# Kernel tuning notes

Hardware: AMD Instinct MI355X
Metric: run time of the kernel (lower is better)

The kernel has to match this reference:

```python
import jax, jax.numpy as jnp
import numpy as np

H, W, C_IN, C_OUT, N = 512, 512, 256, 256, 65536


def setup_inputs() -> dict:
    key = jax.random.key(0)
    k1, k2, k3, k4 = jax.random.split(key, 4)
    feature = jax.random.normal(k1, (1, C_IN, H, W), dtype=jnp.float32)
    weight = jax.random.normal(k2, (C_OUT, C_IN, 3, 3), dtype=jnp.float32) * 0.05
    # base sparse locations in the unpadded map; build 3x3 neighborhood indices
    # into the PADDED ([H+2, W+2]) map, exactly like F.pad + fancy indexing.
    base_h = jax.random.randint(k3, (N,), 0, H, dtype=jnp.int32)
    base_w = jax.random.randint(k4, (N,), 0, W, dtype=jnp.int32)
    dh = jnp.repeat(jnp.arange(3, dtype=jnp.int32), 3)  # [9]: 0,0,0,1,1,1,2,2,2
    dw = jnp.tile(jnp.arange(3, dtype=jnp.int32), 3)    # [9]: 0,1,2,0,1,2,...
    h_idx = base_h[None, :] + dh[:, None]  # [9, N], values in [0, H+1]
    w_idx = base_w[None, :] + dw[:, None]  # [9, N], values in [0, W+1]
    return {"feature": feature, "weight": weight, "h_idx": h_idx, "w_idx": w_idx}


def reference(feature, weight, h_idx, w_idx):
    # feature: [1, C, H, W]; weight: [Cout, C, 3, 3]; h_idx/w_idx: [9, N]
    C = feature.shape[1]
    out_ch = weight.shape[0]
    # F.pad(feature, [1,1,1,1])[0] -> [C, H+2, W+2]
    padded = jnp.pad(feature, ((0, 0), (0, 0), (1, 1), (1, 1)))[0]
    # gather 3x3 neighborhoods at sparse locations -> [C, 9, N]
    gathered = padded[:, h_idx, w_idx]
    # .view(9*C, -1): contiguous reshape gives row index c*9 + k
    g = gathered.reshape(C * 9, -1)  # [C*9, N]
    # kernel_d2s = weight.view(out, -1): row ordering c*9 + (kh*3+kw) matches
    k2d = weight.reshape(out_ch, -1)  # [Cout, C*9]
    return k2d @ g  # [Cout, N]
```

## Files before the change

kernel.cpp:

```cpp
#include <hip/hip_runtime.h>
#include <hip/hip_bf16.h>

#define HH 512
#define WW 512
#define CIN 256
#define COUT 256
#define NPTS 65536
#define PW 514
#define NPIX (PW * PW)
#define NKT 72

typedef __bf16 bf16x8 __attribute__((ext_vector_type(8)));
typedef float f32x16 __attribute__((ext_vector_type(16)));
typedef unsigned short us8 __attribute__((ext_vector_type(8)));

static __device__ __forceinline__ unsigned short f2bf(float f) {
  unsigned u = __builtin_bit_cast(unsigned, f);
  unsigned r = u + 0x7fffu + ((u >> 16) & 1u);
  return (unsigned short)(r >> 16);
}

static __device__ __forceinline__ void gload16(const void* g, void* l) {
  __builtin_amdgcn_global_load_lds(
      (const __attribute__((address_space(1))) unsigned int*)g,
      (__attribute__((address_space(3))) unsigned int*)l, 16, 0, 0);
}

__global__ __launch_bounds__(256) void prep_weight(const float* __restrict__ w,
                                                   unsigned short* __restrict__ A) {
  int i = blockIdx.x * 256 + threadIdx.x;
  int kt = i >> 13;
  int o  = i & 8191;
  int r  = o >> 5;
  int cp = (o >> 3) & 3;
  int j  = o & 7;
  int c  = cp ^ ((r >> 1) & 3);
  int k  = kt * 32 + c * 8 + j;
  int t  = k >> 8;
  int ci = k & 255;
  A[i] = f2bf(w[r * 2304 + ci * 9 + t]);
}

__global__ __launch_bounds__(256) void border_zero(unsigned short* __restrict__ Ft) {
  int g = blockIdx.x * 256 + threadIdx.x;
  if (g >= 2052 * 32) return;
  int p = g >> 5, c = g & 31;
  int py, px;
  if (p < 514)        { py = 0;        px = p; }
  else if (p < 1028)  { py = 513;      px = p - 514; }
  else if (p < 1540)  { py = p - 1027; px = 0; }
  else                { py = p - 1539; px = 513; }
  *(us8*)&Ft[((size_t)py * PW + px) * 256 + c * 8] = (us8){0, 0, 0, 0, 0, 0, 0, 0};
}

__global__ __launch_bounds__(256) void transpose_feat(const float* __restrict__ f,
                                                      unsigned short* __restrict__ Ft) {
  __shared__ unsigned short lds[64 * 264];
  int pix0 = blockIdx.x * 64;
  int y = pix0 >> 9, x0 = pix0 & 511;
  int tid = threadIdx.x;
  int p = tid & 63;
  int cb = tid >> 6;
  const float* src = f + pix0 + p;
  for (int c8 = 0; c8 < 8; ++c8) {
    us8 v;
#pragma unroll
    for (int j = 0; j < 8; ++j) {
      int ci = cb * 64 + c8 * 8 + j;
      v[j] = f2bf(src[ci * 262144]);
    }
    *(us8*)&lds[p * 264 + cb * 64 + c8 * 8] = v;
  }
  __syncthreads();
  int cic = tid & 31;
  int pr = tid >> 5;
  for (int g = 0; g < 8; ++g) {
    int p2 = pr + g * 8;
    us8 v = *(const us8*)&lds[p2 * 264 + cic * 8];
    *(us8*)&Ft[((size_t)((y + 1) * PW + x0 + 1 + p2)) * 256 + cic * 8] = v;
  }
}

__global__ __launch_bounds__(512, 2) void gemm_gather(
    const unsigned short* __restrict__ A,
    const unsigned short* __restrict__ Ft,
    const int* __restrict__ hidx,
    const int* __restrict__ widx,
    float* __restrict__ out) {
  __shared__ unsigned short lds[65536];
  unsigned short* ldsB = lds + 32768;

  int tid = threadIdx.x;
  int lane = tid & 63, wv = tid >> 6;
  int wm = wv & 1, wn = wv >> 1;
  int n0 = blockIdx.x << 8;

  int c0 = tid >> 2;
  int cc = (tid & 3) ^ ((tid >> 3) & 3);
  long pixA = (long)hidx[n0 + c0] * PW + widx[n0 + c0];
  long pixB = (long)hidx[n0 + 128 + c0] * PW + widx[n0 + 128 + c0];
  const unsigned short* FtB0 = Ft + pixA * 256 + cc * 8;
  const unsigned short* FtB1 = Ft + pixB * 256 + cc * 8;

#define STAGE_A(kt_)                                                          \
  do {                                                                        \
    const unsigned short* g_ = A + (size_t)(kt_) * 8192 + tid * 8;            \
    unsigned short* l_ = lds + ((kt_) & 3) * 8192 + tid * 8;                  \
    gload16(g_, l_);                                                          \
    gload16(g_ + 4096, l_ + 4096);                                            \
  } while (0)

#define STAGE_B(kt_)                                                          \
  do {                                                                        \
    int tp_ = (kt_) >> 3;                                                     \
    int q_ = tp_ / 3;                                                         \
    long off_ = (long)(q_ * PW + (tp_ - q_ * 3)) * 256 + ((kt_) & 7) * 32;    \
    unsigned short* l_ = ldsB + ((kt_) & 3) * 8192 + tid * 8;                 \
    gload16(FtB0 + off_, l_);                                                 \
    gload16(FtB1 + off_, l_ + 4096);                                          \
  } while (0)

#define LDA(dst, buf_, kg_, mt_)                                              \
  do {                                                                        \
    int r_ = wm * 128 + (mt_) * 32 + (lane & 31);                             \
    int c_ = ((kg_) * 2 + (lane >> 5)) ^ ((r_ >> 1) & 3);                     \
    dst = *(const bf16x8*)&lds[(buf_) * 8192 + r_ * 32 + c_ * 8];             \
  } while (0)

#define LDB(dst, buf_, kg_, nt_)                                              \
  do {                                                                        \
    int col_ = wn * 64 + (nt_) * 32 + (lane & 31);                            \
    int c_ = ((kg_) * 2 + (lane >> 5)) ^ ((col_ >> 1) & 3);                   \
    dst = *(const bf16x8*)&ldsB[(buf_) * 8192 + col_ * 32 + c_ * 8];          \
  } while (0)

#define MFMA8()                                                               \
  do {                                                                        \
    __builtin_amdgcn_s_setprio(1);                                            \
    acc[0][0] = __builtin_amdgcn_mfma_f32_32x32x16_bf16(af0, b0, acc[0][0], 0, 0, 0); \
    acc[0][1] = __builtin_amdgcn_mfma_f32_32x32x16_bf16(af0, b1, acc[0][1], 0, 0, 0); \
    acc[1][0] = __builtin_amdgcn_mfma_f32_32x32x16_bf16(af1, b0, acc[1][0], 0, 0, 0); \
    acc[1][1] = __builtin_amdgcn_mfma_f32_32x32x16_bf16(af1, b1, acc[1][1], 0, 0, 0); \
    acc[2][0] = __builtin_amdgcn_mfma_f32_32x32x16_bf16(af2, b0, acc[2][0], 0, 0, 0); \
    acc[2][1] = __builtin_amdgcn_mfma_f32_32x32x16_bf16(af2, b1, acc[2][1], 0, 0, 0); \
    acc[3][0] = __builtin_amdgcn_mfma_f32_32x32x16_bf16(af3, b0, acc[3][0], 0, 0, 0); \
    acc[3][1] = __builtin_amdgcn_mfma_f32_32x32x16_bf16(af3, b1, acc[3][1], 0, 0, 0); \
    __builtin_amdgcn_s_setprio(0);                                            \
  } while (0)

#define TILE(kt_, DOSTAGE_, WAITN_)                                           \
  do {                                                                        \
    int buf_ = (kt_) & 3;                                                     \
    bf16x8 af0, af1, af2, af3, b0, b1;                                        \
    LDA(af0, buf_, 0, 0); LDA(af1, buf_, 0, 1);                               \
    LDA(af2, buf_, 0, 2); LDA(af3, buf_, 0, 3);                               \
    LDB(b0, buf_, 0, 0); LDB(b1, buf_, 0, 1);                                 \
    if (DOSTAGE_) STAGE_A((kt_) + 3);                                         \
    __builtin_amdgcn_s_barrier();                                             \
    MFMA8();                                                                  \
    __builtin_amdgcn_s_barrier();                                             \
    LDA(af0, buf_, 1, 0); LDA(af1, buf_, 1, 1);                               \
    LDA(af2, buf_, 1, 2); LDA(af3, buf_, 1, 3);                               \
    LDB(b0, buf_, 1, 0); LDB(b1, buf_, 1, 1);                                 \
    if (DOSTAGE_) STAGE_B((kt_) + 3);                                         \
    __builtin_amdgcn_s_barrier();                                             \
    MFMA8();                                                                  \
    if ((WAITN_) == 8) asm volatile("s_waitcnt vmcnt(8)" ::: "memory");       \
    else if ((WAITN_) == 4) asm volatile("s_waitcnt vmcnt(4)" ::: "memory");  \
    else if ((WAITN_) == 0) asm volatile("s_waitcnt vmcnt(0)" ::: "memory");  \
    __builtin_amdgcn_s_barrier();                                             \
  } while (0)

  f32x16 acc[4][2];
#pragma unroll
  for (int mt = 0; mt < 4; ++mt)
#pragma unroll
    for (int nt = 0; nt < 2; ++nt)
      acc[mt][nt] = (f32x16)(0.f);

  STAGE_A(0); STAGE_B(0);
  STAGE_A(1); STAGE_B(1);
  STAGE_A(2); STAGE_B(2);
  asm volatile("s_waitcnt vmcnt(8)" ::: "memory");
  __builtin_amdgcn_s_barrier();

  for (int kt = 0; kt < NKT - 3; ++kt)
    TILE(kt, 1, 8);
  TILE(69, 0, 4);
  TILE(70, 0, 0);
  TILE(71, 0, -1);

#undef STAGE_A
#undef STAGE_B
#undef LDA
#undef LDB
#undef MFMA8
#undef TILE

  int colb = n0 + wn * 64 + (lane & 31);
  int rb = wm * 128 + ((lane >> 5) << 2);
#pragma unroll
  for (int mt = 0; mt < 4; ++mt)
#pragma unroll
    for (int nt = 0; nt < 2; ++nt)
#pragma unroll
      for (int r = 0; r < 16; ++r) {
        int row = rb + mt * 32 + (r & 3) + ((r >> 2) << 3);
        out[(size_t)row * NPTS + colb + nt * 32] = acc[mt][nt][r];
      }
}

__global__ __launch_bounds__(256) void naive_conv(const float* __restrict__ f,
                                                  const float* __restrict__ w,
                                                  const int* __restrict__ hi,
                                                  const int* __restrict__ wi,
                                                  float* __restrict__ out) {
  int idx = blockIdx.x * 256 + threadIdx.x;
  int n = idx & (NPTS - 1);
  int co = idx >> 16;
  int bh = hi[n] - 1;
  int bw = wi[n] - 1;
  float acc = 0.f;
  for (int ci = 0; ci < CIN; ++ci) {
    const float* fc = f + (size_t)ci * 262144;
    const float* wc = w + (size_t)co * 2304 + ci * 9;
#pragma unroll
    for (int t = 0; t < 9; ++t) {
      int y = bh + t / 3, x = bw + t % 3;
      float v = (y >= 0 && y < 512 && x >= 0 && x < 512) ? fc[y * 512 + x] : 0.f;
      acc += wc[t] * v;
    }
  }
  out[(size_t)co * NPTS + n] = acc;
}

extern "C" void kernel_launch(void* const* d_in, const int* in_sizes, int n_in,
                              void* d_out, int out_size, void* d_ws, size_t ws_size,
                              hipStream_t stream) {
  const float* feature = (const float*)d_in[0];
  const float* weight  = (const float*)d_in[1];
  const int* hidx      = (const int*)d_in[2];
  const int* widx      = (const int*)d_in[3];
  float* out           = (float*)d_out;

  const size_t FT_OFF = 2ull * 1024 * 1024;
  const size_t FT_BYTES = (size_t)NPIX * 256 * 2;
  const size_t NEED = FT_OFF + FT_BYTES;

  if (ws_size >= NEED) {
    unsigned short* Abf = (unsigned short*)d_ws;
    unsigned short* Ft = (unsigned short*)((char*)d_ws + FT_OFF);
    prep_weight<<<(NKT * 8192) / 256, 256, 0, stream>>>(weight, Abf);
    border_zero<<<(2052 * 32 + 255) / 256, 256, 0, stream>>>(Ft);
    transpose_feat<<<262144 / 64, 256, 0, stream>>>(feature, Ft);
    gemm_gather<<<NPTS / 256, 512, 0, stream>>>(Abf, Ft, hidx, widx, out);
  } else {
    naive_conv<<<(COUT * NPTS) / 256, 256, 0, stream>>>(feature, weight, hidx, widx, out);
  }
}
```

Measured before the change: 177.7 us.

## Restructure gather-GEMM pipeline with wider B stages and single barrier per tile

```diff
diff --git a/kernel.cpp b/kernel.cpp
--- a/kernel.cpp
+++ b/kernel.cpp
@@ -87,89 +87,93 @@
     const int* __restrict__ hidx,
     const int* __restrict__ widx,
     float* __restrict__ out) {
-  __shared__ unsigned short lds[65536];
-  unsigned short* ldsB = lds + 32768;
+  __shared__ unsigned short lds[73728];
+  unsigned short* ldsB = lds + 24576;
 
   int tid = threadIdx.x;
   int lane = tid & 63, wv = tid >> 6;
   int wm = wv & 1, wn = wv >> 1;
   int n0 = blockIdx.x << 8;
 
-  int c0 = tid >> 2;
-  int cc = (tid & 3) ^ ((tid >> 3) & 3);
-  long pixA = (long)hidx[n0 + c0] * PW + widx[n0 + c0];
-  long pixB = (long)hidx[n0 + 128 + c0] * PW + widx[n0 + 128 + c0];
-  const unsigned short* FtB0 = Ft + pixA * 256 + cc * 8;
-  const unsigned short* FtB1 = Ft + pixB * 256 + cc * 8;
-
-#define STAGE_A(kt_)                                                          \
-  do {                                                                        \
-    const unsigned short* g_ = A + (size_t)(kt_) * 8192 + tid * 8;            \
-    unsigned short* l_ = lds + ((kt_) & 3) * 8192 + tid * 8;                  \
+  int lcB = (tid & 7) ^ ((tid >> 3) & 7);
+  const unsigned short* FtQ0;
+  const unsigned short* FtQ1;
+  const unsigned short* FtQ2;
+  const unsigned short* FtQ3;
+  {
+    int cq = tid >> 3;
+    FtQ0 = Ft + (long)(hidx[n0 + cq] * PW + widx[n0 + cq]) * 256 + lcB * 8;
+    FtQ1 = Ft + (long)(hidx[n0 + 64 + cq] * PW + widx[n0 + 64 + cq]) * 256 + lcB * 8;
+    FtQ2 = Ft + (long)(hidx[n0 + 128 + cq] * PW + widx[n0 + 128 + cq]) * 256 + lcB * 8;
+    FtQ3 = Ft + (long)(hidx[n0 + 192 + cq] * PW + widx[n0 + 192 + cq]) * 256 + lcB * 8;
+  }
+
+#define STAGE_A(t_, ab_)                                                      \
+  do {                                                                        \
+    const unsigned short* g_ = A + (size_t)(t_) * 8192 + tid * 8;             \
+    unsigned short* l_ = lds + (ab_) * 8192 + tid * 8;                        \
     gload16(g_, l_);                                                          \
     gload16(g_ + 4096, l_ + 4096);                                            \
   } while (0)
 
-#define STAGE_B(kt_)                                                          \
-  do {                                                                        \
-    int tp_ = (kt_) >> 3;                                                     \
-    int q_ = tp_ / 3;                                                         \
-    long off_ = (long)(q_ * PW + (tp_ - q_ * 3)) * 256 + ((kt_) & 7) * 32;    \
-    unsigned short* l_ = ldsB + ((kt_) & 3) * 8192 + tid * 8;                 \
-    gload16(FtB0 + off_, l_);                                                 \
-    gload16(FtB1 + off_, l_ + 4096);                                          \
-  } while (0)
-
-#define LDA(dst, buf_, kg_, mt_)                                              \
+#define STAGE_B(p_, bb_)                                                      \
+  do {                                                                        \
+    int tap_ = (p_) >> 2;                                                     \
+    long off_ = (long)((tap_ / 3) * PW + (tap_ - (tap_ / 3) * 3)) * 256 +     \
+                ((p_) & 3) * 64;                                              \
+    unsigned short* l_ = ldsB + (bb_) * 16384 + tid * 8;                      \
+    gload16(FtQ0 + off_, l_);                                                 \
+    gload16(FtQ1 + off_, l_ + 4096);                                          \
+    gload16(FtQ2 + off_, l_ + 8192);                                          \
+    gload16(FtQ3 + off_, l_ + 12288);                                         \
+  } while (0)
+
+#define LDA(dst, ab_, kg_, mt_)                                               \
   do {                                                                        \
     int r_ = wm * 128 + (mt_) * 32 + (lane & 31);                             \
     int c_ = ((kg_) * 2 + (lane >> 5)) ^ ((r_ >> 1) & 3);                     \
-    dst = *(const bf16x8*)&lds[(buf_) * 8192 + r_ * 32 + c_ * 8];             \
-  } while (0)
-
-#define LDB(dst, buf_, kg_, nt_)                                              \
+    dst = *(const bf16x8*)&lds[(ab_) * 8192 + r_ * 32 + c_ * 8];              \
+  } while (0)
+
+#define LDB(dst, bb_, s_, kg_, nt_)                                           \
   do {                                                                        \
     int col_ = wn * 64 + (nt_) * 32 + (lane & 31);                            \
-    int c_ = ((kg_) * 2 + (lane >> 5)) ^ ((col_ >> 1) & 3);                   \
-    dst = *(const bf16x8*)&ldsB[(buf_) * 8192 + col_ * 32 + c_ * 8];          \
-  } while (0)
-
-#define MFMA8()                                                               \
+    int pc_ = ((s_) * 4 + (kg_) * 2 + (lane >> 5)) ^ (col_ & 7);              \
+    dst = *(const bf16x8*)&ldsB[(bb_) * 16384 + col_ * 64 + pc_ * 8];         \
+  } while (0)
+
+#define MFMA8(a0, a1, a2, a3, b0, b1)                                         \
   do {                                                                        \
     __builtin_amdgcn_s_setprio(1);                                            \
-    acc[0][0] = __builtin_amdgcn_mfma_f32_32x32x16_bf16(af0, b0, acc[0][0], 0, 0, 0); \
-    acc[0][1] = __builtin_amdgcn_mfma_f32_32x32x16_bf16(af0, b1, acc[0][1], 0, 0, 0); \
-    acc[1][0] = __builtin_amdgcn_mfma_f32_32x32x16_bf16(af1, b0, acc[1][0], 0, 0, 0); \
-    acc[1][1] = __builtin_amdgcn_mfma_f32_32x32x16_bf16(af1, b1, acc[1][1], 0, 0, 0); \
-    acc[2][0] = __builtin_amdgcn_mfma_f32_32x32x16_bf16(af2, b0, acc[2][0], 0, 0, 0); \
-    acc[2][1] = __builtin_amdgcn_mfma_f32_32x32x16_bf16(af2, b1, acc[2][1], 0, 0, 0); \
-    acc[3][0] = __builtin_amdgcn_mfma_f32_32x32x16_bf16(af3, b0, acc[3][0], 0, 0, 0); \
-    acc[3][1] = __builtin_amdgcn_mfma_f32_32x32x16_bf16(af3, b1, acc[3][1], 0, 0, 0); \
+    acc[0][0] = __builtin_amdgcn_mfma_f32_32x32x16_bf16(a0, b0, acc[0][0], 0, 0, 0); \
+    acc[0][1] = __builtin_amdgcn_mfma_f32_32x32x16_bf16(a0, b1, acc[0][1], 0, 0, 0); \
+    acc[1][0] = __builtin_amdgcn_mfma_f32_32x32x16_bf16(a1, b0, acc[1][0], 0, 0, 0); \
+    acc[1][1] = __builtin_amdgcn_mfma_f32_32x32x16_bf16(a1, b1, acc[1][1], 0, 0, 0); \
+    acc[2][0] = __builtin_amdgcn_mfma_f32_32x32x16_bf16(a2, b0, acc[2][0], 0, 0, 0); \
+    acc[2][1] = __builtin_amdgcn_mfma_f32_32x32x16_bf16(a2, b1, acc[2][1], 0, 0, 0); \
+    acc[3][0] = __builtin_amdgcn_mfma_f32_32x32x16_bf16(a3, b0, acc[3][0], 0, 0, 0); \
+    acc[3][1] = __builtin_amdgcn_mfma_f32_32x32x16_bf16(a3, b1, acc[3][1], 0, 0, 0); \
     __builtin_amdgcn_s_setprio(0);                                            \
   } while (0)
 
-#define TILE(kt_, DOSTAGE_, WAITN_)                                           \
-  do {                                                                        \
-    int buf_ = (kt_) & 3;                                                     \
-    bf16x8 af0, af1, af2, af3, b0, b1;                                        \
-    LDA(af0, buf_, 0, 0); LDA(af1, buf_, 0, 1);                               \
-    LDA(af2, buf_, 0, 2); LDA(af3, buf_, 0, 3);                               \
-    LDB(b0, buf_, 0, 0); LDB(b1, buf_, 0, 1);                                 \
-    if (DOSTAGE_) STAGE_A((kt_) + 3);                                         \
+#define HEAD(W_)                                                              \
+  do {                                                                        \
+    asm volatile("s_waitcnt lgkmcnt(0)" ::: "memory");                        \
+    asm volatile("s_waitcnt vmcnt(" #W_ ")" ::: "memory");                    \
     __builtin_amdgcn_s_barrier();                                             \
-    MFMA8();                                                                  \
-    __builtin_amdgcn_s_barrier();                                             \
-    LDA(af0, buf_, 1, 0); LDA(af1, buf_, 1, 1);                               \
-    LDA(af2, buf_, 1, 2); LDA(af3, buf_, 1, 3);                               \
-    LDB(b0, buf_, 1, 0); LDB(b1, buf_, 1, 1);                                 \
-    if (DOSTAGE_) STAGE_B((kt_) + 3);                                         \
-    __builtin_amdgcn_s_barrier();                                             \
-    MFMA8();                                                                  \
-    if ((WAITN_) == 8) asm volatile("s_waitcnt vmcnt(8)" ::: "memory");       \
-    else if ((WAITN_) == 4) asm volatile("s_waitcnt vmcnt(4)" ::: "memory");  \
-    else if ((WAITN_) == 0) asm volatile("s_waitcnt vmcnt(0)" ::: "memory");  \
-    __builtin_amdgcn_s_barrier();                                             \
-  } while (0)
+    __builtin_amdgcn_sched_barrier(0);                                        \
+  } while (0)
+
+#define TILE_BODY(ab_, bb_, s_)                                               \
+  bf16x8 xa0, xa1, xa2, xa3, xb0, xb1, ya0, ya1, ya2, ya3, yb0, yb1;          \
+  LDA(xa0, ab_, 0, 0); LDA(xa1, ab_, 0, 1); LDA(xa2, ab_, 0, 2);              \
+  LDA(xa3, ab_, 0, 3); LDB(xb0, bb_, s_, 0, 0); LDB(xb1, bb_, s_, 0, 1)
+
+#define TILE_TAIL(ab_, bb_, s_)                                               \
+  LDA(ya0, ab_, 1, 0); LDA(ya1, ab_, 1, 1); LDA(ya2, ab_, 1, 2);              \
+  LDA(ya3, ab_, 1, 3); LDB(yb0, bb_, s_, 1, 0); LDB(yb1, bb_, s_, 1, 1);      \
+  MFMA8(xa0, xa1, xa2, xa3, xb0, xb1);                                        \
+  MFMA8(ya0, ya1, ya2, ya3, yb0, yb1)
 
   f32x16 acc[4][2];
 #pragma unroll
@@ -178,24 +182,63 @@
     for (int nt = 0; nt < 2; ++nt)
       acc[mt][nt] = (f32x16)(0.f);
 
-  STAGE_A(0); STAGE_B(0);
-  STAGE_A(1); STAGE_B(1);
-  STAGE_A(2); STAGE_B(2);
-  asm volatile("s_waitcnt vmcnt(8)" ::: "memory");
-  __builtin_amdgcn_s_barrier();
-
-  for (int kt = 0; kt < NKT - 3; ++kt)
-    TILE(kt, 1, 8);
-  TILE(69, 0, 4);
-  TILE(70, 0, 0);
-  TILE(71, 0, -1);
+  STAGE_A(0, 0);
+  STAGE_B(0, 0);
+  STAGE_A(1, 1);
+  STAGE_B(1, 1);
+
+  int abE = 0, bbP = 0;
+  for (int p = 0; p < 34; ++p) {
+    int abO = abE + 1; if (abO == 3) abO = 0;
+    int abN = abO + 1; if (abN == 3) abN = 0;
+    int bbN = bbP + 2; if (bbN >= 3) bbN -= 3;
+    {
+      HEAD(6);
+      TILE_BODY(abE, bbP, 0);
+      STAGE_A(2 * p + 2, abN);
+      STAGE_B(p + 2, bbN);
+      TILE_TAIL(abE, bbP, 0);
+    }
+    {
+      HEAD(6);
+      TILE_BODY(abO, bbP, 1);
+      STAGE_A(2 * p + 3, abE);
+      TILE_TAIL(abO, bbP, 1);
+    }
+    abE = abN;
+    bbP = bbP + 1; if (bbP == 3) bbP = 0;
+  }
+  {
+    HEAD(6);
+    TILE_BODY(2, 1, 0);
+    STAGE_A(70, 1);
+    TILE_TAIL(2, 1, 0);
+  }
+  {
+    HEAD(2);
+    TILE_BODY(0, 1, 1);
+    STAGE_A(71, 2);
+    TILE_TAIL(0, 1, 1);
+  }
+  {
+    HEAD(2);
+    TILE_BODY(1, 2, 0);
+    TILE_TAIL(1, 2, 0);
+  }
+  {
+    HEAD(0);
+    TILE_BODY(2, 2, 1);
+    TILE_TAIL(2, 2, 1);
+  }
 
 #undef STAGE_A
 #undef STAGE_B
 #undef LDA
 #undef LDB
 #undef MFMA8
-#undef TILE
+#undef HEAD
+#undef TILE_BODY
+#undef TILE_TAIL
 
   int colb = n0 + wn * 64 + (lane & 31);
   int rb = wm * 128 + ((lane >> 5) << 2);
```

After: 173.8 us. -2.2%, faster.
